# Kernel tuning notes

Hardware: AMD Instinct MI355X
Metric: run time of the kernel (lower is better)

Reference implementation:

```python
import jax, jax.numpy as jnp
import numpy as np

EPS = 1e-9
ROUTING_ITERATIONS = 3


def setup_inputs() -> dict:
    key = jax.random.key(0)
    k1, k2 = jax.random.split(key)
    B, Nin, Din = 32, 2048, 16   # batch, input capsules, input capsule dim
    Nout, Dout = 64, 32          # output capsules, output capsule dim
    x = jax.random.normal(k1, (B, Nin, Din), dtype=jnp.float32)
    # transformation weights W[i, j, d, k] (shared across batch)
    W = jax.random.normal(k2, (Nin, Nout, Dout, Din), dtype=jnp.float32) * 0.05
    bias = jnp.zeros((Nout, Dout), dtype=jnp.float32)
    return {"x": x, "W": W, "bias": bias}


def _squash(s):
    # squash along last axis (capsule vector dim)
    sq_norm = jnp.sum(jnp.square(s), axis=-1, keepdims=True)
    scale = sq_norm / (1.0 + sq_norm)
    return scale * s / jnp.sqrt(sq_norm + EPS)


def reference(x, W, bias):
    # u_hat[b,i,j,d] = sum_k W[i,j,d,k] * x[b,i,k]
    u_hat = jnp.einsum('ijdk,bik->bijd', W, x)
    B, Nin, Nout, Dout = u_hat.shape
    b_log = jnp.zeros((B, Nin, Nout), dtype=u_hat.dtype)  # routing logits
    v = None
    for it in range(ROUTING_ITERATIONS):
        c = jax.nn.softmax(b_log, axis=2)                 # coupling coeffs over Nout
        s = jnp.einsum('bij,bijd->bjd', c, u_hat) + bias  # [B, Nout, Dout]
        v = _squash(s)
        if it < ROUTING_ITERATIONS - 1:
            b_log = b_log + jnp.einsum('bijd,bjd->bij', u_hat, v)
    return v  # [B, Nout, Dout]
```

## Files before the change

kernel.cpp:

```cpp
#include <hip/hip_runtime.h>
#include <hip/hip_bf16.h>
#include <stdint.h>


#define CB    32
#define NIN   2048
#define DIN   16
#define NOUT  64
#define DOUT  32
#define IPB   8
#define NCB   (NIN / IPB)
#define WI    (NOUT * DOUT * DIN)
#define WELEM ((size_t)NIN * WI)

typedef __attribute__((ext_vector_type(8)))  short bf16x8;
typedef __attribute__((ext_vector_type(16))) float f32x16;
typedef _Float16 h2 __attribute__((ext_vector_type(2)));

#define XOFF_IT 67584
#define SMEM_IT 77824
#define SMEM_P0 10240

static __device__ __forceinline__ uint32_t pack_bf2(float a, float b) {
    __hip_bfloat162 hh = __float22bfloat162_rn(make_float2(a, b));
    uint32_t u; __builtin_memcpy(&u, &hh, 4); return u;
}
static __device__ __forceinline__ uint16_t f2bf(float v) {
    return (uint16_t)(pack_bf2(v, 0.f) & 0xffffu);
}
static __device__ __forceinline__ float bf2f(uint16_t u) {
    uint32_t v = (uint32_t)u << 16; float f; __builtin_memcpy(&f, &v, 4); return f;
}
static __device__ __forceinline__ uint32_t pack_h2(float a, float b) {
    h2 r; r.x = (_Float16)a; r.y = (_Float16)b;
    uint32_t u; __builtin_memcpy(&u, &r, 4); return u;
}
static __device__ __forceinline__ h2 as_h2(uint32_t u) {
    h2 r; __builtin_memcpy(&r, &u, 4); return r;
}
static __device__ __forceinline__ float bflo(uint32_t u) {
    uint32_t v = u << 16; float f; __builtin_memcpy(&f, &v, 4); return f;
}
static __device__ __forceinline__ float bfhi(uint32_t u) {
    uint32_t v = u & 0xffff0000u; float f; __builtin_memcpy(&f, &v, 4); return f;
}

__global__ __launch_bounds__(1024, 4) void caps_pass0(
    const float* __restrict__ x, const float* __restrict__ Wf,
    uint32_t* __restrict__ WhOut, uint16_t* __restrict__ s_partial)
{
    extern __shared__ char smem[];
    uint32_t* x_lds = (uint32_t*)smem;

    const int cb = blockIdx.x;
    const int t  = threadIdx.x;
    const int w  = t >> 6, l = t & 63;
    const int bl = l & 31, h = l >> 5;
    const int j0 = w * 4;

    {
        const int b = t >> 5, i = (t >> 2) & 7, k4 = (t & 3) * 4;
        const float4 xv = *(const float4*)(x + ((size_t)b * NIN + cb * IPB + i) * DIN + k4);
        x_lds[(i * 32 + b) * 10 + (k4 >> 1)]     = pack_bf2(xv.x, xv.y);
        x_lds[(i * 32 + b) * 10 + (k4 >> 1) + 1] = pack_bf2(xv.z, xv.w);
    }
    __syncthreads();

    f32x16 sacc[4];
#pragma unroll
    for (int jj = 0; jj < 4; ++jj) sacc[jj] = (f32x16)0.0f;

#pragma unroll 1
    for (int i = 0; i < IPB; ++i) {
        const size_t wbase = (size_t)(cb * IPB + i) * WI;
        bf16x8 bfr;
        {
            uint32_t uu[4];
            const uint32_t* xp = &x_lds[(i * 32 + bl) * 10 + h * 4];
            uu[0] = xp[0]; uu[1] = xp[1]; uu[2] = xp[2]; uu[3] = xp[3];
            __builtin_memcpy(&bfr, uu, 16);
        }
#pragma unroll
        for (int jj = 0; jj < 4; ++jj) {
            const int j = j0 + jj;
            const size_t eoff = wbase + (size_t)(j * 32 + bl) * 16 + h * 8;
            const float4* wp = (const float4*)(Wf + eoff);
            const float4 a4 = wp[0], b4 = wp[1];
            uint32_t uu[4];
            uu[0] = pack_bf2(a4.x, a4.y); uu[1] = pack_bf2(a4.z, a4.w);
            uu[2] = pack_bf2(b4.x, b4.y); uu[3] = pack_bf2(b4.z, b4.w);
            bf16x8 afr; __builtin_memcpy(&afr, uu, 16);
            uint4 st; st.x = uu[0]; st.y = uu[1]; st.z = uu[2]; st.w = uu[3];
            *(uint4*)(WhOut + (eoff >> 1)) = st;
            sacc[jj] = __builtin_amdgcn_mfma_f32_32x32x16_bf16(afr, bfr, sacc[jj], 0, 0, 0);
        }
    }

#pragma unroll
    for (int jj = 0; jj < 4; ++jj) {
        const int j = j0 + jj;
#pragma unroll
        for (int r = 0; r < 16; ++r) {
            const int d = (r & 3) + 8 * (r >> 2) + 4 * h;
            s_partial[(size_t)cb * (2048 * 32) + (size_t)(j * 32 + d) * 32 + bl] =
                f2bf(sacc[jj][r] * (1.0f / 64.0f));
        }
    }
}

template <int IT>
__global__ __launch_bounds__(1024, 4) void caps_it(
    const float* __restrict__ x, const uint16_t* __restrict__ Wh,
    const float* __restrict__ v_prev, const float* __restrict__ blog_in,
    float* __restrict__ blog_out, uint16_t* __restrict__ s_partial)
{
    extern __shared__ char smem[];
    float*    c_lds = (float*)smem;
    uint32_t* x_lds = (uint32_t*)(smem + XOFF_IT);

    const int cb = blockIdx.x;
    const int t  = threadIdx.x;
    const int w  = t >> 6, l = t & 63;
    const int bl = l & 31, h = l >> 5;
    const int j0 = w * 4;

    {
        const int b = t >> 5, i = (t >> 2) & 7, k4 = (t & 3) * 4;
        const float4 xv = *(const float4*)(x + ((size_t)b * NIN + cb * IPB + i) * DIN + k4);
        x_lds[(i * 32 + b) * 10 + (k4 >> 1)]     = pack_bf2(xv.x, xv.y);
        x_lds[(i * 32 + b) * 10 + (k4 >> 1) + 1] = pack_bf2(xv.z, xv.w);
    }

    constexpr int base_dp[8] = {0, 1, 4, 5, 8, 9, 12, 13};
    uint32_t vreg[4][8];
#pragma unroll
    for (int jj = 0; jj < 4; ++jj)
#pragma unroll
        for (int rp = 0; rp < 8; ++rp) {
            const int d0 = 2 * (base_dp[rp] + 2 * h);
            const float2 vv = *(const float2*)(v_prev
                + ((size_t)bl * NOUT + j0 + jj) * DOUT + d0);
            vreg[jj][rp] = pack_h2(vv.x, vv.y);
        }
    __syncthreads();

#pragma unroll 2
    for (int i = 0; i < IPB; ++i) {
        const size_t wbase = (size_t)(cb * IPB + i) * WI;
        bf16x8 bfr;
        {
            uint32_t uu[4];
            const uint32_t* xp = &x_lds[(i * 32 + bl) * 10 + h * 4];
            uu[0] = xp[0]; uu[1] = xp[1]; uu[2] = xp[2]; uu[3] = xp[3];
            __builtin_memcpy(&bfr, uu, 16);
        }
#pragma unroll
        for (int jj = 0; jj < 4; ++jj) {
            const int j = j0 + jj;
            const bf16x8 afr = *(const bf16x8*)(Wh + wbase + (size_t)(j * 32 + bl) * 16 + h * 8);
            const f32x16 D = __builtin_amdgcn_mfma_f32_32x32x16_bf16(afr, bfr, (f32x16)0.0f, 0, 0, 0);
            float acc = 0.f;
#pragma unroll
            for (int rp = 0; rp < 8; ++rp) {
                h2 dpk; dpk.x = (_Float16)D[2 * rp]; dpk.y = (_Float16)D[2 * rp + 1];
                acc = __builtin_amdgcn_fdot2(dpk, as_h2(vreg[jj][rp]), acc, false);
            }
            acc += __shfl_xor(acc, 32);
            if (h == 0) c_lds[(i * 64 + j) * 33 + bl] = acc;
        }
    }
    __syncthreads();

#pragma unroll 1
    for (int q = 0; q < 16; ++q) {
        const int row = w * 16 + q;
        const int i = row >> 5, b = row & 31;
        const int ig = cb * IPB + i;
        float bv = c_lds[(i * 64 + l) * 33 + b];
        if (IT == 2) bv += blog_in[((size_t)b * NIN + ig) * NOUT + l];
        if (IT == 1) blog_out[((size_t)b * NIN + ig) * NOUT + l] = bv;
        float m = bv;
#pragma unroll
        for (int o = 32; o; o >>= 1) m = fmaxf(m, __shfl_xor(m, o));
        const float e = __expf(bv - m);
        float s = e;
#pragma unroll
        for (int o = 32; o; o >>= 1) s += __shfl_xor(s, o);
        c_lds[(i * 64 + l) * 33 + b] = e / s;
    }
    __syncthreads();

    f32x16 sacc[4];
#pragma unroll
    for (int jj = 0; jj < 4; ++jj) sacc[jj] = (f32x16)0.0f;

#pragma unroll 2
    for (int i = 0; i < IPB; ++i) {
        const size_t wbase = (size_t)(cb * IPB + i) * WI;
        uint32_t xu[4];
        {
            const uint32_t* xp = &x_lds[(i * 32 + bl) * 10 + h * 4];
            xu[0] = xp[0]; xu[1] = xp[1]; xu[2] = xp[2]; xu[3] = xp[3];
        }
#pragma unroll
        for (int jj = 0; jj < 4; ++jj) {
            const int j = j0 + jj;
            const bf16x8 afr = *(const bf16x8*)(Wh + wbase + (size_t)(j * 32 + bl) * 16 + h * 8);
            const float cv = c_lds[(i * 64 + j) * 33 + bl];
            uint32_t cu[4];
#pragma unroll
            for (int q = 0; q < 4; ++q)
                cu[q] = pack_bf2(bflo(xu[q]) * cv, bfhi(xu[q]) * cv);
            bf16x8 cxf; __builtin_memcpy(&cxf, cu, 16);
            sacc[jj] = __builtin_amdgcn_mfma_f32_32x32x16_bf16(afr, cxf, sacc[jj], 0, 0, 0);
        }
    }

#pragma unroll
    for (int jj = 0; jj < 4; ++jj) {
        const int j = j0 + jj;
#pragma unroll
        for (int r = 0; r < 16; ++r) {
            const int d = (r & 3) + 8 * (r >> 2) + 4 * h;
            s_partial[(size_t)cb * (2048 * 32) + (size_t)(j * 32 + d) * 32 + bl] =
                f2bf(sacc[jj][r]);
        }
    }
}

__global__ __launch_bounds__(256) void caps_squash(
    const uint16_t* __restrict__ sp, const float* __restrict__ bias,
    float* __restrict__ vout)
{
    const int j  = blockIdx.x >> 2;
    const int bq = blockIdx.x & 3;
    const int t  = threadIdx.x;
    const int d  = t >> 3;
    const int blq = t & 7;
    const int b  = bq * 8 + blq;

    const uint16_t* p = sp + (size_t)(j * 32 + d) * 32 + b;
    float s0 = 0.f, s1 = 0.f, s2 = 0.f, s3 = 0.f;
#pragma unroll 4
    for (int c = 0; c < NCB; c += 4) {
        s0 += bf2f(p[(size_t)(c + 0) * (2048 * 32)]);
        s1 += bf2f(p[(size_t)(c + 1) * (2048 * 32)]);
        s2 += bf2f(p[(size_t)(c + 2) * (2048 * 32)]);
        s3 += bf2f(p[(size_t)(c + 3) * (2048 * 32)]);
    }
    const float sv = ((s0 + s1) + (s2 + s3)) + bias[j * DOUT + d];

    float sq = sv * sv;
    sq += __shfl_xor(sq, 8);
    sq += __shfl_xor(sq, 16);
    sq += __shfl_xor(sq, 32);

    __shared__ float sh[4][8];
    if ((t & 63) < 8) sh[t >> 6][t & 7] = sq;
    __syncthreads();
    const float tot = sh[0][blq] + sh[1][blq] + sh[2][blq] + sh[3][blq];
    const float scale = (tot / (1.0f + tot)) * rsqrtf(tot + 1e-9f);
    vout[(size_t)b * (NOUT * DOUT) + j * DOUT + d] = scale * sv;
}

extern "C" void kernel_launch(void* const* d_in, const int* in_sizes, int n_in,
                              void* d_out, int out_size, void* d_ws, size_t ws_size,
                              hipStream_t stream) {
    const float* x    = (const float*)d_in[0];
    const float* W    = (const float*)d_in[1];
    const float* bias = (const float*)d_in[2];
    float* out = (float*)d_out;

    char* base = (char*)d_ws;
    uint32_t* Wh    = (uint32_t*)base;
    float*    blog  = (float*)(base + WELEM * 2);
    uint16_t* spart = (uint16_t*)(base + WELEM * 2 + (size_t)CB * NIN * NOUT * 4);
    float*    vbuf  = (float*)(base + WELEM * 2 + (size_t)CB * NIN * NOUT * 4
                               + (size_t)NCB * 2048 * 32 * 2);
    (void)ws_size;

    hipFuncSetAttribute(reinterpret_cast<const void*>(caps_pass0),
                        hipFuncAttributeMaxDynamicSharedMemorySize, SMEM_P0);
    hipFuncSetAttribute(reinterpret_cast<const void*>(caps_it<1>),
                        hipFuncAttributeMaxDynamicSharedMemorySize, SMEM_IT);
    hipFuncSetAttribute(reinterpret_cast<const void*>(caps_it<2>),
                        hipFuncAttributeMaxDynamicSharedMemorySize, SMEM_IT);

    caps_pass0<<<NCB, 1024, SMEM_P0, stream>>>(x, W, (uint32_t*)Wh, spart);
    caps_squash<<<NOUT * 4, 256, 0, stream>>>(spart, bias, vbuf);

    caps_it<1><<<NCB, 1024, SMEM_IT, stream>>>(x, (const uint16_t*)Wh, vbuf, nullptr, blog, spart);
    caps_squash<<<NOUT * 4, 256, 0, stream>>>(spart, bias, vbuf);

    caps_it<2><<<NCB, 1024, SMEM_IT, stream>>>(x, (const uint16_t*)Wh, vbuf, blog, nullptr, spart);
    caps_squash<<<NOUT * 4, 256, 0, stream>>>(spart, bias, out);
}
```

Before: 261.8 us.

## Fuse routing phases per input capsule with double-buffered coupling LDS

The three phases of each routing iteration (agreement logits, softmax over output capsules, weighted accumulation) now run per input capsule in one loop, instead of as three separate passes over all eight capsules. The coupling buffer holds only two capsules at a time, which cuts the LDS footprint from about 77KB to 27KB. The W tile and x fragment can then be reused while still fresh rather than reloaded in a second pass. In exchange each iteration adds two block-wide barriers, and launch bounds drop the min-blocks hint from 4 to 1, which changes register allocation.

```diff
diff --git a/kernel.cpp b/kernel.cpp
--- a/kernel.cpp
+++ b/kernel.cpp
@@ -17,8 +17,9 @@
 typedef __attribute__((ext_vector_type(16))) float f32x16;
 typedef _Float16 h2 __attribute__((ext_vector_type(2)));
 
-#define XOFF_IT 67584
-#define SMEM_IT 77824
+#define CSTRIDE 2112
+#define XOFF_IT 16896
+#define SMEM_IT 27136
 #define SMEM_P0 10240
 
 static __device__ __forceinline__ uint32_t pack_bf2(float a, float b) {
@@ -45,7 +46,7 @@
     uint32_t v = u & 0xffff0000u; float f; __builtin_memcpy(&f, &v, 4); return f;
 }
 
-__global__ __launch_bounds__(1024, 4) void caps_pass0(
+__global__ __launch_bounds__(1024, 1) void caps_pass0(
     const float* __restrict__ x, const float* __restrict__ Wf,
     uint32_t* __restrict__ WhOut, uint16_t* __restrict__ s_partial)
 {
@@ -109,7 +110,7 @@
 }
 
 template <int IT>
-__global__ __launch_bounds__(1024, 4) void caps_it(
+__global__ __launch_bounds__(1024, 1) void caps_it(
     const float* __restrict__ x, const uint16_t* __restrict__ Wh,
     const float* __restrict__ v_prev, const float* __restrict__ blog_in,
     float* __restrict__ blog_out, uint16_t* __restrict__ s_partial)
@@ -144,16 +145,23 @@
         }
     __syncthreads();
 
-#pragma unroll 2
+    f32x16 sacc[4];
+#pragma unroll
+    for (int jj = 0; jj < 4; ++jj) sacc[jj] = (f32x16)0.0f;
+
+#pragma unroll 1
     for (int i = 0; i < IPB; ++i) {
-        const size_t wbase = (size_t)(cb * IPB + i) * WI;
-        bf16x8 bfr;
+        const int p = (i & 1) * CSTRIDE;
+        const int ig = cb * IPB + i;
+        const size_t wbase = (size_t)ig * WI;
+
+        uint32_t xu[4];
         {
-            uint32_t uu[4];
             const uint32_t* xp = &x_lds[(i * 32 + bl) * 10 + h * 4];
-            uu[0] = xp[0]; uu[1] = xp[1]; uu[2] = xp[2]; uu[3] = xp[3];
-            __builtin_memcpy(&bfr, uu, 16);
-        }
+            xu[0] = xp[0]; xu[1] = xp[1]; xu[2] = xp[2]; xu[3] = xp[3];
+        }
+        bf16x8 bfr; __builtin_memcpy(&bfr, xu, 16);
+
 #pragma unroll
         for (int jj = 0; jj < 4; ++jj) {
             const int j = j0 + jj;
@@ -166,52 +174,37 @@
                 acc = __builtin_amdgcn_fdot2(dpk, as_h2(vreg[jj][rp]), acc, false);
             }
             acc += __shfl_xor(acc, 32);
-            if (h == 0) c_lds[(i * 64 + j) * 33 + bl] = acc;
-        }
-    }
-    __syncthreads();
-
-#pragma unroll 1
-    for (int q = 0; q < 16; ++q) {
-        const int row = w * 16 + q;
-        const int i = row >> 5, b = row & 31;
-        const int ig = cb * IPB + i;
-        float bv = c_lds[(i * 64 + l) * 33 + b];
-        if (IT == 2) bv += blog_in[((size_t)b * NIN + ig) * NOUT + l];
-        if (IT == 1) blog_out[((size_t)b * NIN + ig) * NOUT + l] = bv;
-        float m = bv;
-#pragma unroll
-        for (int o = 32; o; o >>= 1) m = fmaxf(m, __shfl_xor(m, o));
-        const float e = __expf(bv - m);
-        float s = e;
-#pragma unroll
-        for (int o = 32; o; o >>= 1) s += __shfl_xor(s, o);
-        c_lds[(i * 64 + l) * 33 + b] = e / s;
-    }
-    __syncthreads();
-
-    f32x16 sacc[4];
-#pragma unroll
-    for (int jj = 0; jj < 4; ++jj) sacc[jj] = (f32x16)0.0f;
-
-#pragma unroll 2
-    for (int i = 0; i < IPB; ++i) {
-        const size_t wbase = (size_t)(cb * IPB + i) * WI;
-        uint32_t xu[4];
-        {
-            const uint32_t* xp = &x_lds[(i * 32 + bl) * 10 + h * 4];
-            xu[0] = xp[0]; xu[1] = xp[1]; xu[2] = xp[2]; xu[3] = xp[3];
-        }
+            if (h == 0) c_lds[p + j * 33 + bl] = acc;
+        }
+        __syncthreads();
+
+#pragma unroll
+        for (int rr = 0; rr < 2; ++rr) {
+            const int b = w * 2 + rr;
+            float bv = c_lds[p + l * 33 + b];
+            if (IT == 2) bv += blog_in[((size_t)b * NIN + ig) * NOUT + l];
+            if (IT == 1) blog_out[((size_t)b * NIN + ig) * NOUT + l] = bv;
+            float m = bv;
+#pragma unroll
+            for (int o = 32; o; o >>= 1) m = fmaxf(m, __shfl_xor(m, o));
+            const float e = __expf(bv - m);
+            float s = e;
+#pragma unroll
+            for (int o = 32; o; o >>= 1) s += __shfl_xor(s, o);
+            c_lds[p + l * 33 + b] = e / s;
+        }
+        __syncthreads();
+
 #pragma unroll
         for (int jj = 0; jj < 4; ++jj) {
             const int j = j0 + jj;
-            const bf16x8 afr = *(const bf16x8*)(Wh + wbase + (size_t)(j * 32 + bl) * 16 + h * 8);
-            const float cv = c_lds[(i * 64 + j) * 33 + bl];
+            const float cv = c_lds[p + j * 33 + bl];
             uint32_t cu[4];
 #pragma unroll
             for (int q = 0; q < 4; ++q)
                 cu[q] = pack_bf2(bflo(xu[q]) * cv, bfhi(xu[q]) * cv);
             bf16x8 cxf; __builtin_memcpy(&cxf, cu, 16);
+            const bf16x8 afr = *(const bf16x8*)(Wh + wbase + (size_t)(j * 32 + bl) * 16 + h * 8);
             sacc[jj] = __builtin_amdgcn_mfma_f32_32x32x16_bf16(afr, cxf, sacc[jj], 0, 0, 0);
         }
     }
```

Result: slower. 373.7 us (+42.7%).
